# Kernel optimization log

Measured on AMD Instinct MI355X. Metric: run time of the kernel, lower is better.

The kernel has to match this reference:

```python
import jax, jax.numpy as jnp
import numpy as np

B, N, NSAMPLE = 8, 2048, 32
D = 64          # input feature channels
C1, C2 = 64, 128  # MLP channels (channels list after +3 on input: 67 -> 64 -> 128)
RADIUS = 0.15
EPS = 1e-5


def setup_inputs() -> dict:
    key = jax.random.key(0)
    ks = jax.random.split(key, 4)
    position = jax.random.uniform(ks[0], (B, N, 3), dtype=jnp.float32)
    feature = jax.random.normal(ks[1], (B, N, D), dtype=jnp.float32)
    W1 = jax.random.normal(ks[2], (D + 3, C1), dtype=jnp.float32) * 0.05
    gamma1 = jnp.ones((C1,), jnp.float32)
    beta1 = jnp.zeros((C1,), jnp.float32)
    W2 = jax.random.normal(ks[3], (C1, C2), dtype=jnp.float32) * 0.05
    gamma2 = jnp.ones((C2,), jnp.float32)
    beta2 = jnp.zeros((C2,), jnp.float32)
    return {"position": position, "feature": feature,
            "W1": W1, "gamma1": gamma1, "beta1": beta1,
            "W2": W2, "gamma2": gamma2, "beta2": beta2}


def _ball_query(xyz, radius, nsample):
    # squared pairwise distances [B, N, N]
    sq = (jnp.sum(xyz ** 2, -1)[:, :, None]
          + jnp.sum(xyz ** 2, -1)[:, None, :]
          - 2.0 * jnp.einsum('bnc,bmc->bnm', xyz, xyz))
    n = xyz.shape[1]
    idx = jnp.where(sq > radius ** 2, n, jnp.arange(n, dtype=jnp.int32)[None, None, :])
    idx = jnp.sort(idx, axis=-1)[:, :, :nsample]            # [B, N, nsample]
    first = idx[:, :, :1]
    return jnp.where(idx == n, first, idx)                  # pad misses with first neighbor


def _gather(points, idx):
    # points [B, N, C], idx [B, S, K] -> [B, S, K, C]
    b, s, k = idx.shape
    flat = jnp.take_along_axis(points, idx.reshape(b, s * k, 1), axis=1)
    return flat.reshape(b, s, k, points.shape[-1])


def _bn_relu(x, gamma, beta, relu=True):
    # BatchNorm1d over channel dim (train-mode stats across B*N*S), per linearblock
    mean = jnp.mean(x, axis=(0, 1, 2), keepdims=True)
    var = jnp.var(x, axis=(0, 1, 2), keepdims=True)
    y = (x - mean) * jax.lax.rsqrt(var + EPS) * gamma + beta
    return jax.nn.relu(y) if relu else y


def reference(position, feature, W1, gamma1, beta1, W2, gamma2, beta2):
    b, n, _ = position.shape
    idx = _ball_query(position, RADIUS, NSAMPLE)            # [B, N, nsample]
    grouped_xyz = _gather(position, idx) - position[:, :, None, :]  # [B,N,ns,3]
    grouped_feat = _gather(feature, idx)                    # [B, N, ns, D]
    h = jnp.concatenate([grouped_xyz, grouped_feat], axis=-1)  # [B, N, ns, 3+D]
    h = _bn_relu(h @ W1, gamma1, beta1)                     # [B, N, ns, C1]
    h = _bn_relu(h @ W2, gamma2, beta2)                     # [B, N, ns, C2]
    new_feature = jnp.max(h, axis=2)                        # [B, N, C2]
    return position, new_feature
```

## Files before the change

kernel.cpp:

```cpp
#include <hip/hip_runtime.h>
#include <hip/hip_bf16.h>


#define BB 8
#define NN 2048
#define KK 32
#define DD 64
#define CC1 64
#define CC2 128
#define TOTROWS (BB*NN*KK)
#define SITES (BB*NN)
#define PSLICES 256
#define DBLOCKS 1024

typedef __bf16 bf16x8 __attribute__((ext_vector_type(8)));
typedef float  f32x4  __attribute__((ext_vector_type(4)));

__device__ __forceinline__ void lds_add(float* p, float v) {
  __hip_atomic_fetch_add(p, v, __ATOMIC_RELAXED, __HIP_MEMORY_SCOPE_WORKGROUP);
}

__global__ __launch_bounds__(1024, 1) void kQ_ball_scatter(
    const float* __restrict__ pos, int* __restrict__ idx,
    float* __restrict__ Pc, float* __restrict__ Px,
    float* __restrict__ Py, float* __restrict__ Pz,
    float* __restrict__ momP)
{
  __shared__ float4 P[NN];
  __shared__ unsigned int Sc[NN], Sx[NN], Sy[NN], Sz[NN];
  __shared__ int idxL[64*KK];
  __shared__ float mred[16*9];
  const int b = blockIdx.x >> 5;
  const int slice = blockIdx.x & 31;
  for (int i = threadIdx.x; i < NN; i += 1024) {
    const float* p = pos + ((size_t)b*NN + i)*3;
    float x = p[0], y = p[1], z = p[2];
    float s = __fadd_rn(__fadd_rn(__fmul_rn(x,x), __fmul_rn(y,y)), __fmul_rn(z,z));
    P[i] = make_float4(x, y, z, s);
    Sc[i] = 0u; Sx[i] = 0u; Sy[i] = 0u; Sz[i] = 0u;
  }
  __syncthreads();
  const int wave = threadIdx.x >> 6, lane = threadIdx.x & 63;
  const float R2 = (float)(0.15 * 0.15);
  const unsigned long long lt = (lane == 63) ? 0x7fffffffffffffffull
                                             : ((1ull << lane) - 1ull);
  for (int qi = wave; qi < 64; qi += 16) {
    const int q = slice*64 + qi;
    const float4 Q = P[q];
    int* ip = idx + ((size_t)b*NN + q)*KK;
    int* il = idxL + qi*KK;
    int cnt = 0, first = -1;
    for (int step = 0; step < 32; ++step) {
      float4 p = P[step*64 + lane];
      float d = __fmul_rn(Q.x, p.x);
      d = fmaf(Q.y, p.y, d);
      d = fmaf(Q.z, p.z, d);
      float sq = __fsub_rn(__fadd_rn(Q.w, p.w), __fmul_rn(2.0f, d));
      bool in = !(sq > R2);
      unsigned long long mask = __ballot(in);
      if (first < 0 && mask) first = step*64 + (int)__builtin_ctzll(mask);
      int dst = cnt + (int)__popcll(mask & lt);
      if (in && dst < KK) { ip[dst] = step*64 + lane; il[dst] = step*64 + lane; }
      cnt += (int)__popcll(mask);
      if (cnt >= KK) break;
    }
    if (lane >= cnt && lane < KK) { ip[lane] = first; il[lane] = first; }
  }
  __syncthreads();
  const int sl = threadIdx.x >> 4;
  const int kg = threadIdx.x & 15;
  const int ip0 = idxL[sl*KK];
  const float4 C = P[slice*64 + sl];
  const float FS = 4194304.0f;
  float m1x=0.f,m1y=0.f,m1z=0.f,mxx=0.f,myy=0.f,mzz=0.f,mxy=0.f,mxz=0.f,myz=0.f;
  int wt = 0;
  #pragma unroll
  for (int j = 0; j < 2; ++j) {
    const int k = kg*2 + j;
    const int m = idxL[sl*KK + k];
    const float4 Pm = P[m];
    float dx = Pm.x - C.x;
    float dy = Pm.y - C.y;
    float dz = Pm.z - C.z;
    if (k > 0 && m == ip0) {
      ++wt;
    } else {
      atomicAdd(&Sc[m], 1u);
      atomicAdd(&Sx[m], (unsigned int)__float2int_rn(dx*FS));
      atomicAdd(&Sy[m], (unsigned int)__float2int_rn(dy*FS));
      atomicAdd(&Sz[m], (unsigned int)__float2int_rn(dz*FS));
    }
    m1x += dx; m1y += dy; m1z += dz;
    mxx = fmaf(dx,dx,mxx); myy = fmaf(dy,dy,myy); mzz = fmaf(dz,dz,mzz);
    mxy = fmaf(dx,dy,mxy); mxz = fmaf(dx,dz,mxz); myz = fmaf(dy,dz,myz);
  }
  if (wt > 0) {
    const float4 P0 = P[ip0];
    float dx0 = P0.x - C.x;
    float dy0 = P0.y - C.y;
    float dz0 = P0.z - C.z;
    atomicAdd(&Sc[ip0], (unsigned int)wt);
    atomicAdd(&Sx[ip0], (unsigned int)(wt*__float2int_rn(dx0*FS)));
    atomicAdd(&Sy[ip0], (unsigned int)(wt*__float2int_rn(dy0*FS)));
    atomicAdd(&Sz[ip0], (unsigned int)(wt*__float2int_rn(dz0*FS)));
  }
  const int wv = threadIdx.x >> 6;
  float vals[9] = {m1x,m1y,m1z,mxx,myy,mzz,mxy,mxz,myz};
  #pragma unroll
  for (int i = 0; i < 9; ++i) {
    float v = vals[i];
    #pragma unroll
    for (int s = 1; s < 64; s <<= 1) v += __shfl_xor(v, s, 64);
    if (lane == 0) mred[wv*9 + i] = v;
  }
  __syncthreads();
  const float IS = 2.38418579101562500e-7f;
  float* pc = Pc + (size_t)blockIdx.x*NN;
  float* px = Px + (size_t)blockIdx.x*NN;
  float* py = Py + (size_t)blockIdx.x*NN;
  float* pz = Pz + (size_t)blockIdx.x*NN;
  for (int i = threadIdx.x; i < NN; i += 1024) {
    pc[i] = (float)Sc[i];
    px[i] = (float)(int)Sx[i] * IS;
    py[i] = (float)(int)Sy[i] * IS;
    pz[i] = (float)(int)Sz[i] * IS;
  }
  if (threadIdx.x < 9) {
    float s = 0.f;
    #pragma unroll
    for (int w2 = 0; w2 < 16; ++w2) s += mred[w2*9 + threadIdx.x];
    momP[(size_t)blockIdx.x*16 + threadIdx.x] = s;
  }
}

__global__ __launch_bounds__(256) void kB_g(const float* __restrict__ feat,
                                            const float* __restrict__ W1,
                                            const float* __restrict__ Pc,
                                            const float* __restrict__ Px,
                                            const float* __restrict__ Py,
                                            const float* __restrict__ Pz,
                                            float* __restrict__ g,
                                            float* __restrict__ A_p)
{
  __shared__ float red[320];
  __shared__ float cntL[128], dxL[128], dyL[128], dzL[128];
  for (int i = threadIdx.x; i < 320; i += 256) red[i] = 0.f;
  const int row0B = blockIdx.x * 128;
  const int bb = row0B >> 11;
  for (int r2 = threadIdx.x; r2 < 128; r2 += 256) {
    const int m = (row0B + r2) & (NN-1);
    float s0 = 0.f, s1 = 0.f, s2 = 0.f, s3 = 0.f;
    #pragma unroll 4
    for (int q = 0; q < 32; ++q) {
      const size_t base = (size_t)(bb*32 + q)*NN + m;
      s0 += Pc[base]; s1 += Px[base]; s2 += Py[base]; s3 += Pz[base];
    }
    cntL[r2] = s0; dxL[r2] = s1; dyL[r2] = s2; dzL[r2] = s3;
  }
  __syncthreads();
  const int lane = threadIdx.x & 63;
  const int quad = lane >> 4;
  const int col  = lane & 15;
  const int gw = (blockIdx.x*256 + threadIdx.x) >> 6;

  bf16x8 Bf[2][4];
  #pragma unroll
  for (int kt = 0; kt < 2; ++kt)
    #pragma unroll
    for (int nt = 0; nt < 4; ++nt) {
      bf16x8 v;
      #pragma unroll
      for (int j = 0; j < 8; ++j)
        v[j] = (__bf16)W1[(3 + kt*32 + quad*8 + j)*CC1 + nt*16 + col];
      Bf[kt][nt] = v;
    }
  float a1[4], a2[4], a3[4], a4[4], a5[4];
  #pragma unroll
  for (int nt = 0; nt < 4; ++nt) { a1[nt]=0.f; a2[nt]=0.f; a3[nt]=0.f; a4[nt]=0.f; a5[nt]=0.f; }

  for (int t = 0; t < 2; ++t) {
    const int row0 = (gw*2 + t) * 16;
    bf16x8 Af[2];
    #pragma unroll
    for (int kt = 0; kt < 2; ++kt) {
      const float4* fp =
        (const float4*)(feat + (size_t)(row0 + col)*DD + kt*32 + quad*8);
      float4 f0 = fp[0], f1 = fp[1];
      float fv[8] = {f0.x,f0.y,f0.z,f0.w,f1.x,f1.y,f1.z,f1.w};
      bf16x8 v;
      #pragma unroll
      for (int j = 0; j < 8; ++j) v[j] = (__bf16)fv[j];
      Af[kt] = v;
    }
    float cw[4], dxw[4], dyw[4], dzw[4];
    #pragma unroll
    for (int r = 0; r < 4; ++r) {
      int rl = row0 - row0B + quad*4 + r;
      cw[r] = cntL[rl]; dxw[r] = dxL[rl]; dyw[r] = dyL[rl]; dzw[r] = dzL[rl];
    }
    #pragma unroll
    for (int nt = 0; nt < 4; ++nt) {
      f32x4 a = {0.f, 0.f, 0.f, 0.f};
      a = __builtin_amdgcn_mfma_f32_16x16x32_bf16(Af[0], Bf[0][nt], a, 0, 0, 0);
      a = __builtin_amdgcn_mfma_f32_16x16x32_bf16(Af[1], Bf[1][nt], a, 0, 0, 0);
      #pragma unroll
      for (int r = 0; r < 4; ++r) {
        float v = a[r];
        g[(size_t)(row0 + quad*4 + r)*CC1 + nt*16 + col] = v;
        float cv = cw[r]*v;
        a1[nt] += cv; a2[nt] = fmaf(cv, v, a2[nt]);
        a3[nt] = fmaf(dxw[r], v, a3[nt]);
        a4[nt] = fmaf(dyw[r], v, a4[nt]);
        a5[nt] = fmaf(dzw[r], v, a5[nt]);
      }
    }
  }
  #pragma unroll
  for (int nt = 0; nt < 4; ++nt) {
    float v1=a1[nt], v2=a2[nt], v3=a3[nt], v4=a4[nt], v5=a5[nt];
    v1 += __shfl_xor(v1,16,64); v1 += __shfl_xor(v1,32,64);
    v2 += __shfl_xor(v2,16,64); v2 += __shfl_xor(v2,32,64);
    v3 += __shfl_xor(v3,16,64); v3 += __shfl_xor(v3,32,64);
    v4 += __shfl_xor(v4,16,64); v4 += __shfl_xor(v4,32,64);
    v5 += __shfl_xor(v5,16,64); v5 += __shfl_xor(v5,32,64);
    if (quad == 0) {
      int ch = nt*16 + col;
      lds_add(&red[ch], v1);
      lds_add(&red[64+ch], v2);
      lds_add(&red[128+ch], v3);
      lds_add(&red[192+ch], v4);
      lds_add(&red[256+ch], v5);
    }
  }
  __syncthreads();
  for (int i = threadIdx.x; i < 320; i += 256)
    A_p[(size_t)blockIdx.x*320 + i] = red[i];
}

__global__ __launch_bounds__(256) void kS_fold(
    const float* __restrict__ W1, const float* __restrict__ gamma1,
    const float* __restrict__ beta1, const float* __restrict__ A_p,
    const float* __restrict__ momP,
    float* __restrict__ sc1, float* __restrict__ sh1, float* __restrict__ W1s)
{
  __shared__ float AL[320];
  __shared__ float mr[256];
  __shared__ float momL[16];
  {
    const int t = threadIdx.x;
    const int i = t & 15, jq = t >> 4;
    float s = 0.f;
    #pragma unroll
    for (int q = 0; q < 16; ++q) s += momP[(size_t)(jq*16 + q)*16 + i];
    mr[t] = s;
  }
  for (int c = threadIdx.x; c < 320; c += 256) {
    float s = 0.f;
    for (int blk = 0; blk < 128; ++blk) s += A_p[(size_t)blk*320 + c];
    AL[c] = s;
  }
  __syncthreads();
  if (threadIdx.x < 16) {
    float tot = 0.f;
    #pragma unroll
    for (int q = 0; q < 16; ++q) tot += mr[q*16 + threadIdx.x];
    momL[threadIdx.x] = tot;
  }
  __syncthreads();
  const int c = threadIdx.x;
  if (c >= CC1) return;
  float wx = W1[c], wy = W1[CC1+c], wz = W1[2*CC1+c];
  float A1 = AL[c], A2 = AL[64+c];
  float A3x = AL[128+c], A3y = AL[192+c], A3z = AL[256+c];
  float sum1 = A1 + wx*momL[0] + wy*momL[1] + wz*momL[2];
  float ss = A2 + 2.f*(wx*A3x + wy*A3y + wz*A3z)
           + wx*wx*momL[3] + wy*wy*momL[4] + wz*wz*momL[5]
           + 2.f*(wx*wy*momL[6] + wx*wz*momL[7] + wy*wz*momL[8]);
  const float invN = 1.0f / (float)TOTROWS;
  float mean = sum1 * invN;
  float var  = ss * invN - mean*mean;
  float sc = rsqrtf(var + 1e-5f) * gamma1[c];
  float sh = beta1[c] - mean * sc;
  sc1[c] = sc; sh1[c] = sh;
  W1s[c] = wx*sc; W1s[64+c] = wy*sc; W1s[128+c] = wz*sc;
}

__global__ __launch_bounds__(256, 2) void kD_mfma(
    const float* __restrict__ pos, const int* __restrict__ idx,
    const float* __restrict__ g, const float* __restrict__ sc1,
    const float* __restrict__ sh1, const float* __restrict__ W1s,
    const float* __restrict__ W2,
    float* __restrict__ stats2P, float* __restrict__ out_nf)
{
  __shared__ __bf16 W2T[CC2*72];
  __shared__ float red2[256];
  red2[threadIdx.x] = 0.f;
  {
    const int n  = threadIdx.x & 127;
    const int k0 = (threadIdx.x >> 7) << 5;
    #pragma unroll
    for (int jj = 0; jj < 4; ++jj) {
      unsigned int pk[4];
      #pragma unroll
      for (int q2 = 0; q2 < 4; ++q2) {
        const int k = k0 + jj*8 + q2*2;
        __bf16 lo = (__bf16)W2[(size_t)k*CC2 + n];
        __bf16 hi = (__bf16)W2[(size_t)(k+1)*CC2 + n];
        unsigned short ulo, uhi;
        __builtin_memcpy(&ulo, &lo, 2);
        __builtin_memcpy(&uhi, &hi, 2);
        pk[q2] = ((unsigned int)uhi << 16) | (unsigned int)ulo;
      }
      __builtin_memcpy(&W2T[n*72 + k0 + jj*8], pk, 16);
    }
  }
  __syncthreads();

  const int lane = threadIdx.x & 63;
  const int quad = lane >> 4;
  const int col  = lane & 15;
  const int wv = (blockIdx.x*256 + threadIdx.x) >> 6;

  float ssum[8], ssq[8];
  #pragma unroll
  for (int nt = 0; nt < 8; ++nt) { ssum[nt] = 0.f; ssq[nt] = 0.f; }

  #pragma clang loop unroll(disable)
  for (int si = 0; si < 4; ++si) {
    const int site = wv*4 + si;
    const int b  = site >> 11;
    const int ls = site & (NN-1);
    const float* pb = pos + (size_t)b*NN*3;
    const int* ip = idx + (size_t)site*KK;

    const int ma = ip[col], mb = ip[16 + col];
    const float ccx = pb[ls*3], ccy = pb[ls*3+1], ccz = pb[ls*3+2];
    const float dxa = pb[ma*3]-ccx, dya = pb[ma*3+1]-ccy, dza = pb[ma*3+2]-ccz;
    const float dxb = pb[mb*3]-ccx, dyb = pb[mb*3+1]-ccy, dzb = pb[mb*3+2]-ccz;

    const float* gbase = g + (size_t)b*NN*CC1;
    const float* ra = gbase + (size_t)ma*CC1 + quad*8;
    const float* rb = gbase + (size_t)mb*CC1 + quad*8;
    f32x4 gA0 = *(const f32x4*)ra,      gA1 = *(const f32x4*)(ra+4);
    f32x4 gA2 = *(const f32x4*)(ra+32), gA3 = *(const f32x4*)(ra+36);
    f32x4 gB0 = *(const f32x4*)rb,      gB1 = *(const f32x4*)(rb+4);
    f32x4 gB2 = *(const f32x4*)(rb+32), gB3 = *(const f32x4*)(rb+36);

    bf16x8 A00, A01, A10, A11;
    {
      const int c0 = quad*8;
      f32x4 x0 = *(const f32x4*)&W1s[c0],     x1 = *(const f32x4*)&W1s[c0+4];
      f32x4 y0 = *(const f32x4*)&W1s[64+c0],  y1 = *(const f32x4*)&W1s[64+c0+4];
      f32x4 z0 = *(const f32x4*)&W1s[128+c0], z1 = *(const f32x4*)&W1s[128+c0+4];
      f32x4 s0 = *(const f32x4*)&sc1[c0],     s1 = *(const f32x4*)&sc1[c0+4];
      f32x4 h0 = *(const f32x4*)&sh1[c0],     h1 = *(const f32x4*)&sh1[c0+4];
      #pragma unroll
      for (int j = 0; j < 8; ++j) {
        float wx = (j<4)?x0[j]:x1[j-4], wy = (j<4)?y0[j]:y1[j-4];
        float wz = (j<4)?z0[j]:z1[j-4], sc = (j<4)?s0[j]:s1[j-4];
        float sh = (j<4)?h0[j]:h1[j-4];
        float ga = (j<4)?gA0[j]:gA1[j-4], gb = (j<4)?gB0[j]:gB1[j-4];
        float ta = fmaf(dza, wz, fmaf(dya, wy, fmaf(dxa, wx, sh)));
        A00[j] = (__bf16)fmaxf(fmaf(ga, sc, ta), 0.f);
        float tb = fmaf(dzb, wz, fmaf(dyb, wy, fmaf(dxb, wx, sh)));
        A10[j] = (__bf16)fmaxf(fmaf(gb, sc, tb), 0.f);
      }
    }
    {
      const int c0 = 32 + quad*8;
      f32x4 x0 = *(const f32x4*)&W1s[c0],     x1 = *(const f32x4*)&W1s[c0+4];
      f32x4 y0 = *(const f32x4*)&W1s[64+c0],  y1 = *(const f32x4*)&W1s[64+c0+4];
      f32x4 z0 = *(const f32x4*)&W1s[128+c0], z1 = *(const f32x4*)&W1s[128+c0+4];
      f32x4 s0 = *(const f32x4*)&sc1[c0],     s1 = *(const f32x4*)&sc1[c0+4];
      f32x4 h0 = *(const f32x4*)&sh1[c0],     h1 = *(const f32x4*)&sh1[c0+4];
      #pragma unroll
      for (int j = 0; j < 8; ++j) {
        float wx = (j<4)?x0[j]:x1[j-4], wy = (j<4)?y0[j]:y1[j-4];
        float wz = (j<4)?z0[j]:z1[j-4], sc = (j<4)?s0[j]:s1[j-4];
        float sh = (j<4)?h0[j]:h1[j-4];
        float ga = (j<4)?gA2[j]:gA3[j-4], gb = (j<4)?gB2[j]:gB3[j-4];
        float ta = fmaf(dza, wz, fmaf(dya, wy, fmaf(dxa, wx, sh)));
        A01[j] = (__bf16)fmaxf(fmaf(ga, sc, ta), 0.f);
        float tb = fmaf(dzb, wz, fmaf(dyb, wy, fmaf(dxb, wx, sh)));
        A11[j] = (__bf16)fmaxf(fmaf(gb, sc, tb), 0.f);
      }
    }

    float* outp = out_nf + (size_t)site*CC2;
    #pragma unroll
    for (int nt = 0; nt < 8; ++nt) {
      const bf16x8 B0 = *(const bf16x8*)&W2T[(nt*16 + col)*72 + quad*8];
      const bf16x8 B1 = *(const bf16x8*)&W2T[(nt*16 + col)*72 + 32 + quad*8];
      float mxv = -3.0e38f;
      f32x4 a = {0.f, 0.f, 0.f, 0.f};
      a = __builtin_amdgcn_mfma_f32_16x16x32_bf16(A00, B0, a, 0, 0, 0);
      a = __builtin_amdgcn_mfma_f32_16x16x32_bf16(A01, B1, a, 0, 0, 0);
      #pragma unroll
      for (int r = 0; r < 4; ++r) {
        float v = a[r];
        ssum[nt] += v; ssq[nt] = fmaf(v, v, ssq[nt]); mxv = fmaxf(mxv, v);
      }
      f32x4 a2 = {0.f, 0.f, 0.f, 0.f};
      a2 = __builtin_amdgcn_mfma_f32_16x16x32_bf16(A10, B0, a2, 0, 0, 0);
      a2 = __builtin_amdgcn_mfma_f32_16x16x32_bf16(A11, B1, a2, 0, 0, 0);
      #pragma unroll
      for (int r = 0; r < 4; ++r) {
        float v = a2[r];
        ssum[nt] += v; ssq[nt] = fmaf(v, v, ssq[nt]); mxv = fmaxf(mxv, v);
      }
      mxv = fmaxf(mxv, __shfl_xor(mxv, 16, 64));
      mxv = fmaxf(mxv, __shfl_xor(mxv, 32, 64));
      if ((nt & 3) == quad) outp[nt*16 + col] = mxv;
    }
  }

  #pragma unroll
  for (int nt = 0; nt < 8; ++nt) {
    float s = ssum[nt];
    s += __shfl_xor(s, 16, 64); s += __shfl_xor(s, 32, 64);
    float q = ssq[nt];
    q += __shfl_xor(q, 16, 64); q += __shfl_xor(q, 32, 64);
    if (lane < 16) {
      atomicAdd(&red2[nt*16 + col], s);
      atomicAdd(&red2[128 + nt*16 + col], q);
    }
  }
  __syncthreads();
  stats2P[(size_t)blockIdx.x*256 + threadIdx.x] = red2[threadIdx.x];
}

__global__ __launch_bounds__(256) void kR2_stats(
    const float* __restrict__ stats2P, float* __restrict__ stats2)
{
  __shared__ float r[256];
  const int c = blockIdx.x;
  float s = 0.f;
  for (int i = threadIdx.x; i < DBLOCKS; i += 256)
    s += stats2P[(size_t)i*256 + c];
  r[threadIdx.x] = s;
  __syncthreads();
  for (int off = 128; off > 0; off >>= 1) {
    if (threadIdx.x < off) r[threadIdx.x] += r[threadIdx.x + off];
    __syncthreads();
  }
  if (threadIdx.x == 0) stats2[c] = r[0];
}

__global__ __launch_bounds__(256) void k45_epi(const float* __restrict__ pos,
                                               const float* __restrict__ g2,
                                               const float* __restrict__ be2,
                                               const float* __restrict__ stats2,
                                               float* __restrict__ out)
{
  int i = blockIdx.x*256 + threadIdx.x;
  if (blockIdx.x < 192) { out[i] = pos[i]; return; }
  int j = i - 192*256;
  int c = j & (CC2-1);
  const float invc = 1.0f / (float)TOTROWS;
  float mean = stats2[c] * invc;
  float var  = stats2[128 + c] * invc - mean*mean;
  float sc = rsqrtf(var + 1e-5f) * g2[c];
  float sh = be2[c] - mean * sc;
  float* out_nf = out + (size_t)BB*NN*3;
  float x = out_nf[j];
  out_nf[j] = fmaxf(fmaf(x, sc, sh), 0.f);
}

extern "C" void kernel_launch(void* const* d_in, const int* in_sizes, int n_in,
                              void* d_out, int out_size, void* d_ws, size_t ws_size,
                              hipStream_t stream) {
  const float* pos  = (const float*)d_in[0];
  const float* feat = (const float*)d_in[1];
  const float* W1   = (const float*)d_in[2];
  const float* g1   = (const float*)d_in[3];
  const float* be1  = (const float*)d_in[4];
  const float* W2   = (const float*)d_in[5];
  const float* g2   = (const float*)d_in[6];
  const float* be2  = (const float*)d_in[7];
  float* out = (float*)d_out;
  float* out_nf = out + (size_t)BB*NN*3;

  char* w = (char*)d_ws;
  int*   idx    = (int*)w;
  float* stats2 = (float*)(w + 0x200000);
  float* sc1    = stats2 + 256;
  float* sh1    = sc1 + 64;
  float* W1s    = sh1 + 64;
  float* A_p    = (float*)(w + 0x210000);
  float* momP   = (float*)(w + 0x250000);
  float* Pc     = (float*)(w + 0x260000);
  float* Px     = Pc + (size_t)PSLICES*NN;
  float* Py     = Px + (size_t)PSLICES*NN;
  float* Pz     = Py + (size_t)PSLICES*NN;
  float* stats2P= (float*)(w + 0x660000);
  float* g      = (float*)(w + 0xA60000);

  kQ_ball_scatter<<<256, 1024, 0, stream>>>(pos, idx, Pc, Px, Py, Pz, momP);
  kB_g      <<<128, 256, 0, stream>>>(feat, W1, Pc, Px, Py, Pz, g, A_p);
  kS_fold   <<<1, 256, 0, stream>>>(W1, g1, be1, A_p, momP, sc1, sh1, W1s);
  kD_mfma   <<<DBLOCKS, 256, 0, stream>>>(pos, idx, g, sc1, sh1, W1s, W2,
                                          stats2P, out_nf);
  kR2_stats <<<256, 256, 0, stream>>>(stats2P, stats2);
  k45_epi   <<<192 + (SITES*CC2)/256, 256, 0, stream>>>(pos, g2, be2, stats2, out);
}
```

Baseline: 173.6 us.

## Fold BN reduction kernels into consumers and move position copy into ball query

Removes the single-block kS_fold kernel by having every kD_mfma block redundantly reduce A_p and momP and compute the layer-1 BN scale/shift into LDS. It also removes kR2_stats: each epilogue block re-reduces all 1024 stats2P partials itself, then applies BN2+ReLU with float4 accesses. The position passthrough copy moves into kQ_ball_scatter. This cuts two launches and their serial dependencies, but each block now does redundant global reads of the partial sums (about 40K floats per kD block and 256K per epilogue block).

```diff
diff --git a/kernel.cpp b/kernel.cpp
--- a/kernel.cpp
+++ b/kernel.cpp
@@ -24,7 +24,7 @@
     const float* __restrict__ pos, int* __restrict__ idx,
     float* __restrict__ Pc, float* __restrict__ Px,
     float* __restrict__ Py, float* __restrict__ Pz,
-    float* __restrict__ momP)
+    float* __restrict__ momP, float* __restrict__ out)
 {
   __shared__ float4 P[NN];
   __shared__ unsigned int Sc[NN], Sx[NN], Sy[NN], Sz[NN];
@@ -131,6 +131,8 @@
     for (int w2 = 0; w2 < 16; ++w2) s += mred[w2*9 + threadIdx.x];
     momP[(size_t)blockIdx.x*16 + threadIdx.x] = s;
   }
+  if (threadIdx.x < 192)
+    out[blockIdx.x*192 + threadIdx.x] = pos[blockIdx.x*192 + threadIdx.x];
 }
 
 __global__ __launch_bounds__(256) void kB_g(const float* __restrict__ feat,
@@ -237,63 +239,21 @@
     A_p[(size_t)blockIdx.x*320 + i] = red[i];
 }
 
-__global__ __launch_bounds__(256) void kS_fold(
-    const float* __restrict__ W1, const float* __restrict__ gamma1,
-    const float* __restrict__ beta1, const float* __restrict__ A_p,
-    const float* __restrict__ momP,
-    float* __restrict__ sc1, float* __restrict__ sh1, float* __restrict__ W1s)
-{
-  __shared__ float AL[320];
-  __shared__ float mr[256];
-  __shared__ float momL[16];
-  {
-    const int t = threadIdx.x;
-    const int i = t & 15, jq = t >> 4;
-    float s = 0.f;
-    #pragma unroll
-    for (int q = 0; q < 16; ++q) s += momP[(size_t)(jq*16 + q)*16 + i];
-    mr[t] = s;
-  }
-  for (int c = threadIdx.x; c < 320; c += 256) {
-    float s = 0.f;
-    for (int blk = 0; blk < 128; ++blk) s += A_p[(size_t)blk*320 + c];
-    AL[c] = s;
-  }
-  __syncthreads();
-  if (threadIdx.x < 16) {
-    float tot = 0.f;
-    #pragma unroll
-    for (int q = 0; q < 16; ++q) tot += mr[q*16 + threadIdx.x];
-    momL[threadIdx.x] = tot;
-  }
-  __syncthreads();
-  const int c = threadIdx.x;
-  if (c >= CC1) return;
-  float wx = W1[c], wy = W1[CC1+c], wz = W1[2*CC1+c];
-  float A1 = AL[c], A2 = AL[64+c];
-  float A3x = AL[128+c], A3y = AL[192+c], A3z = AL[256+c];
-  float sum1 = A1 + wx*momL[0] + wy*momL[1] + wz*momL[2];
-  float ss = A2 + 2.f*(wx*A3x + wy*A3y + wz*A3z)
-           + wx*wx*momL[3] + wy*wy*momL[4] + wz*wz*momL[5]
-           + 2.f*(wx*wy*momL[6] + wx*wz*momL[7] + wy*wz*momL[8]);
-  const float invN = 1.0f / (float)TOTROWS;
-  float mean = sum1 * invN;
-  float var  = ss * invN - mean*mean;
-  float sc = rsqrtf(var + 1e-5f) * gamma1[c];
-  float sh = beta1[c] - mean * sc;
-  sc1[c] = sc; sh1[c] = sh;
-  W1s[c] = wx*sc; W1s[64+c] = wy*sc; W1s[128+c] = wz*sc;
-}
-
 __global__ __launch_bounds__(256, 2) void kD_mfma(
     const float* __restrict__ pos, const int* __restrict__ idx,
-    const float* __restrict__ g, const float* __restrict__ sc1,
-    const float* __restrict__ sh1, const float* __restrict__ W1s,
+    const float* __restrict__ g, const float* __restrict__ A_p,
+    const float* __restrict__ momP, const float* __restrict__ W1,
+    const float* __restrict__ gamma1, const float* __restrict__ beta1,
     const float* __restrict__ W2,
     float* __restrict__ stats2P, float* __restrict__ out_nf)
 {
   __shared__ __bf16 W2T[CC2*72];
   __shared__ float red2[256];
+  __shared__ alignas(16) float AL[320];
+  __shared__ float momL[16];
+  __shared__ alignas(16) float sc1L[64];
+  __shared__ alignas(16) float sh1L[64];
+  __shared__ alignas(16) float W1sL[192];
   red2[threadIdx.x] = 0.f;
   {
     const int n  = threadIdx.x & 127;
@@ -314,6 +274,34 @@
       __builtin_memcpy(&W2T[n*72 + k0 + jj*8], pk, 16);
     }
   }
+  for (int c = threadIdx.x; c < 320; c += 256) {
+    float s = 0.f;
+    for (int blk = 0; blk < 128; ++blk) s += A_p[(size_t)blk*320 + c];
+    AL[c] = s;
+  }
+  if (threadIdx.x < 16) {
+    float s = 0.f;
+    for (int q = 0; q < PSLICES; ++q) s += momP[(size_t)q*16 + threadIdx.x];
+    momL[threadIdx.x] = s;
+  }
+  __syncthreads();
+  if (threadIdx.x < CC1) {
+    const int c = threadIdx.x;
+    float wx = W1[c], wy = W1[CC1+c], wz = W1[2*CC1+c];
+    float A1 = AL[c], A2 = AL[64+c];
+    float A3x = AL[128+c], A3y = AL[192+c], A3z = AL[256+c];
+    float sum1 = A1 + wx*momL[0] + wy*momL[1] + wz*momL[2];
+    float ss = A2 + 2.f*(wx*A3x + wy*A3y + wz*A3z)
+             + wx*wx*momL[3] + wy*wy*momL[4] + wz*wz*momL[5]
+             + 2.f*(wx*wy*momL[6] + wx*wz*momL[7] + wy*wz*momL[8]);
+    const float invN = 1.0f / (float)TOTROWS;
+    float mean = sum1 * invN;
+    float var  = ss * invN - mean*mean;
+    float sc = rsqrtf(var + 1e-5f) * gamma1[c];
+    float sh = beta1[c] - mean * sc;
+    sc1L[c] = sc; sh1L[c] = sh;
+    W1sL[c] = wx*sc; W1sL[64+c] = wy*sc; W1sL[128+c] = wz*sc;
+  }
   __syncthreads();
 
   const int lane = threadIdx.x & 63;
@@ -349,11 +337,11 @@
     bf16x8 A00, A01, A10, A11;
     {
       const int c0 = quad*8;
-      f32x4 x0 = *(const f32x4*)&W1s[c0],     x1 = *(const f32x4*)&W1s[c0+4];
-      f32x4 y0 = *(const f32x4*)&W1s[64+c0],  y1 = *(const f32x4*)&W1s[64+c0+4];
-      f32x4 z0 = *(const f32x4*)&W1s[128+c0], z1 = *(const f32x4*)&W1s[128+c0+4];
-      f32x4 s0 = *(const f32x4*)&sc1[c0],     s1 = *(const f32x4*)&sc1[c0+4];
-      f32x4 h0 = *(const f32x4*)&sh1[c0],     h1 = *(const f32x4*)&sh1[c0+4];
+      f32x4 x0 = *(const f32x4*)&W1sL[c0],     x1 = *(const f32x4*)&W1sL[c0+4];
+      f32x4 y0 = *(const f32x4*)&W1sL[64+c0],  y1 = *(const f32x4*)&W1sL[64+c0+4];
+      f32x4 z0 = *(const f32x4*)&W1sL[128+c0], z1 = *(const f32x4*)&W1sL[128+c0+4];
+      f32x4 s0 = *(const f32x4*)&sc1L[c0],     s1 = *(const f32x4*)&sc1L[c0+4];
+      f32x4 h0 = *(const f32x4*)&sh1L[c0],     h1 = *(const f32x4*)&sh1L[c0+4];
       #pragma unroll
       for (int j = 0; j < 8; ++j) {
         float wx = (j<4)?x0[j]:x1[j-4], wy = (j<4)?y0[j]:y1[j-4];
@@ -368,11 +356,11 @@
     }
     {
       const int c0 = 32 + quad*8;
-      f32x4 x0 = *(const f32x4*)&W1s[c0],     x1 = *(const f32x4*)&W1s[c0+4];
-      f32x4 y0 = *(const f32x4*)&W1s[64+c0],  y1 = *(const f32x4*)&W1s[64+c0+4];
-      f32x4 z0 = *(const f32x4*)&W1s[128+c0], z1 = *(const f32x4*)&W1s[128+c0+4];
-      f32x4 s0 = *(const f32x4*)&sc1[c0],     s1 = *(const f32x4*)&sc1[c0+4];
-      f32x4 h0 = *(const f32x4*)&sh1[c0],     h1 = *(const f32x4*)&sh1[c0+4];
+      f32x4 x0 = *(const f32x4*)&W1sL[c0],     x1 = *(const f32x4*)&W1sL[c0+4];
+      f32x4 y0 = *(const f32x4*)&W1sL[64+c0],  y1 = *(const f32x4*)&W1sL[64+c0+4];
+      f32x4 z0 = *(const f32x4*)&W1sL[128+c0], z1 = *(const f32x4*)&W1sL[128+c0+4];
+      f32x4 s0 = *(const f32x4*)&sc1L[c0],     s1 = *(const f32x4*)&sc1L[c0+4];
+      f32x4 h0 = *(const f32x4*)&sh1L[c0],     h1 = *(const f32x4*)&sh1L[c0+4];
       #pragma unroll
       for (int j = 0; j < 8; ++j) {
         float wx = (j<4)?x0[j]:x1[j-4], wy = (j<4)?y0[j]:y1[j-4];
@@ -429,41 +417,40 @@
   stats2P[(size_t)blockIdx.x*256 + threadIdx.x] = red2[threadIdx.x];
 }
 
-__global__ __launch_bounds__(256) void kR2_stats(
-    const float* __restrict__ stats2P, float* __restrict__ stats2)
+__global__ __launch_bounds__(256) void k45_epi(
+    const float* __restrict__ stats2P, const float* __restrict__ g2,
+    const float* __restrict__ be2, float* __restrict__ out)
 {
-  __shared__ float r[256];
-  const int c = blockIdx.x;
-  float s = 0.f;
-  for (int i = threadIdx.x; i < DBLOCKS; i += 256)
-    s += stats2P[(size_t)i*256 + c];
-  r[threadIdx.x] = s;
-  __syncthreads();
-  for (int off = 128; off > 0; off >>= 1) {
-    if (threadIdx.x < off) r[threadIdx.x] += r[threadIdx.x + off];
-    __syncthreads();
-  }
-  if (threadIdx.x == 0) stats2[c] = r[0];
-}
-
-__global__ __launch_bounds__(256) void k45_epi(const float* __restrict__ pos,
-                                               const float* __restrict__ g2,
-                                               const float* __restrict__ be2,
-                                               const float* __restrict__ stats2,
-                                               float* __restrict__ out)
-{
-  int i = blockIdx.x*256 + threadIdx.x;
-  if (blockIdx.x < 192) { out[i] = pos[i]; return; }
-  int j = i - 192*256;
-  int c = j & (CC2-1);
-  const float invc = 1.0f / (float)TOTROWS;
-  float mean = stats2[c] * invc;
-  float var  = stats2[128 + c] * invc - mean*mean;
-  float sc = rsqrtf(var + 1e-5f) * g2[c];
-  float sh = be2[c] - mean * sc;
+  __shared__ float stF[256];
+  __shared__ float scL[128], shL[128];
+  const int t = threadIdx.x;
+  {
+    float s = 0.f;
+    for (int blk = 0; blk < DBLOCKS; ++blk)
+      s += stats2P[(size_t)blk*256 + t];
+    stF[t] = s;
+  }
+  __syncthreads();
+  if (t < CC2) {
+    const float invc = 1.0f / (float)TOTROWS;
+    float mean = stF[t] * invc;
+    float var  = stF[128 + t] * invc - mean*mean;
+    float sc = rsqrtf(var + 1e-5f) * g2[t];
+    scL[t] = sc; shL[t] = be2[t] - mean * sc;
+  }
+  __syncthreads();
   float* out_nf = out + (size_t)BB*NN*3;
-  float x = out_nf[j];
-  out_nf[j] = fmaxf(fmaf(x, sc, sh), 0.f);
+  float4* o4 = (float4*)out_nf;
+  const size_t e0 = (size_t)blockIdx.x * 2048;
+  for (int e = t; e < 2048; e += 256) {
+    float4 x = o4[e0 + e];
+    const int c = (e << 2) & (CC2-1);
+    x.x = fmaxf(fmaf(x.x, scL[c  ], shL[c  ]), 0.f);
+    x.y = fmaxf(fmaf(x.y, scL[c+1], shL[c+1]), 0.f);
+    x.z = fmaxf(fmaf(x.z, scL[c+2], shL[c+2]), 0.f);
+    x.w = fmaxf(fmaf(x.w, scL[c+3], shL[c+3]), 0.f);
+    o4[e0 + e] = x;
+  }
 }
 
 extern "C" void kernel_launch(void* const* d_in, const int* in_sizes, int n_in,
@@ -482,10 +469,6 @@
 
   char* w = (char*)d_ws;
   int*   idx    = (int*)w;
-  float* stats2 = (float*)(w + 0x200000);
-  float* sc1    = stats2 + 256;
-  float* sh1    = sc1 + 64;
-  float* W1s    = sh1 + 64;
   float* A_p    = (float*)(w + 0x210000);
   float* momP   = (float*)(w + 0x250000);
   float* Pc     = (float*)(w + 0x260000);
@@ -495,11 +478,9 @@
   float* stats2P= (float*)(w + 0x660000);
   float* g      = (float*)(w + 0xA60000);
 
-  kQ_ball_scatter<<<256, 1024, 0, stream>>>(pos, idx, Pc, Px, Py, Pz, momP);
+  kQ_ball_scatter<<<256, 1024, 0, stream>>>(pos, idx, Pc, Px, Py, Pz, momP, out);
   kB_g      <<<128, 256, 0, stream>>>(feat, W1, Pc, Px, Py, Pz, g, A_p);
-  kS_fold   <<<1, 256, 0, stream>>>(W1, g1, be1, A_p, momP, sc1, sh1, W1s);
-  kD_mfma   <<<DBLOCKS, 256, 0, stream>>>(pos, idx, g, sc1, sh1, W1s, W2,
-                                          stats2P, out_nf);
-  kR2_stats <<<256, 256, 0, stream>>>(stats2P, stats2);
-  k45_epi   <<<192 + (SITES*CC2)/256, 256, 0, stream>>>(pos, g2, be2, stats2, out);
-}
+  kD_mfma   <<<DBLOCKS, 256, 0, stream>>>(pos, idx, g, A_p, momP,
+                                          W1, g1, be1, W2, stats2P, out_nf);
+  k45_epi   <<<256, 256, 0, stream>>>(stats2P, g2, be2, out);
+}
```

Measured after the change: 203.3 us. 17.1% more time.

## Fuse BN2 stats reduction into epilogue and move position copy into ball kernel

Applied to the files above, without the earlier changes.

Removes the separate stats-reduction kernel: every epilogue block now reduces all per-block partial stats itself, computes scale/shift into LDS, then applies BN+ReLU with float4 vectorized accesses. The position passthrough copy is moved into the ball-query kernel. This saves a launch and the intermediate stats buffer, but makes each of 256 blocks redundantly read the full 1 MB partial-stats array serially.

```diff
diff --git a/kernel.cpp b/kernel.cpp
--- a/kernel.cpp
+++ b/kernel.cpp
@@ -24,7 +24,7 @@
     const float* __restrict__ pos, int* __restrict__ idx,
     float* __restrict__ Pc, float* __restrict__ Px,
     float* __restrict__ Py, float* __restrict__ Pz,
-    float* __restrict__ momP)
+    float* __restrict__ momP, float* __restrict__ out)
 {
   __shared__ float4 P[NN];
   __shared__ unsigned int Sc[NN], Sx[NN], Sy[NN], Sz[NN];
@@ -131,6 +131,8 @@
     for (int w2 = 0; w2 < 16; ++w2) s += mred[w2*9 + threadIdx.x];
     momP[(size_t)blockIdx.x*16 + threadIdx.x] = s;
   }
+  if (threadIdx.x < 192)
+    out[blockIdx.x*192 + threadIdx.x] = pos[blockIdx.x*192 + threadIdx.x];
 }
 
 __global__ __launch_bounds__(256) void kB_g(const float* __restrict__ feat,
@@ -429,41 +431,40 @@
   stats2P[(size_t)blockIdx.x*256 + threadIdx.x] = red2[threadIdx.x];
 }
 
-__global__ __launch_bounds__(256) void kR2_stats(
-    const float* __restrict__ stats2P, float* __restrict__ stats2)
+__global__ __launch_bounds__(256) void k45_epi(
+    const float* __restrict__ stats2P, const float* __restrict__ g2,
+    const float* __restrict__ be2, float* __restrict__ out)
 {
-  __shared__ float r[256];
-  const int c = blockIdx.x;
-  float s = 0.f;
-  for (int i = threadIdx.x; i < DBLOCKS; i += 256)
-    s += stats2P[(size_t)i*256 + c];
-  r[threadIdx.x] = s;
-  __syncthreads();
-  for (int off = 128; off > 0; off >>= 1) {
-    if (threadIdx.x < off) r[threadIdx.x] += r[threadIdx.x + off];
-    __syncthreads();
-  }
-  if (threadIdx.x == 0) stats2[c] = r[0];
-}
-
-__global__ __launch_bounds__(256) void k45_epi(const float* __restrict__ pos,
-                                               const float* __restrict__ g2,
-                                               const float* __restrict__ be2,
-                                               const float* __restrict__ stats2,
-                                               float* __restrict__ out)
-{
-  int i = blockIdx.x*256 + threadIdx.x;
-  if (blockIdx.x < 192) { out[i] = pos[i]; return; }
-  int j = i - 192*256;
-  int c = j & (CC2-1);
-  const float invc = 1.0f / (float)TOTROWS;
-  float mean = stats2[c] * invc;
-  float var  = stats2[128 + c] * invc - mean*mean;
-  float sc = rsqrtf(var + 1e-5f) * g2[c];
-  float sh = be2[c] - mean * sc;
+  __shared__ float stF[256];
+  __shared__ float scL[128], shL[128];
+  const int t = threadIdx.x;
+  {
+    float s = 0.f;
+    for (int blk = 0; blk < DBLOCKS; ++blk)
+      s += stats2P[(size_t)blk*256 + t];
+    stF[t] = s;
+  }
+  __syncthreads();
+  if (t < CC2) {
+    const float invc = 1.0f / (float)TOTROWS;
+    float mean = stF[t] * invc;
+    float var  = stF[128 + t] * invc - mean*mean;
+    float sc = rsqrtf(var + 1e-5f) * g2[t];
+    scL[t] = sc; shL[t] = be2[t] - mean * sc;
+  }
+  __syncthreads();
   float* out_nf = out + (size_t)BB*NN*3;
-  float x = out_nf[j];
-  out_nf[j] = fmaxf(fmaf(x, sc, sh), 0.f);
+  float4* o4 = (float4*)out_nf;
+  const size_t e0 = (size_t)blockIdx.x * 2048;
+  for (int e = t; e < 2048; e += 256) {
+    float4 x = o4[e0 + e];
+    const int c = (e << 2) & (CC2-1);
+    x.x = fmaxf(fmaf(x.x, scL[c  ], shL[c  ]), 0.f);
+    x.y = fmaxf(fmaf(x.y, scL[c+1], shL[c+1]), 0.f);
+    x.z = fmaxf(fmaf(x.z, scL[c+2], shL[c+2]), 0.f);
+    x.w = fmaxf(fmaf(x.w, scL[c+3], shL[c+3]), 0.f);
+    o4[e0 + e] = x;
+  }
 }
 
 extern "C" void kernel_launch(void* const* d_in, const int* in_sizes, int n_in,
@@ -482,8 +483,7 @@
 
   char* w = (char*)d_ws;
   int*   idx    = (int*)w;
-  float* stats2 = (float*)(w + 0x200000);
-  float* sc1    = stats2 + 256;
+  float* sc1    = (float*)(w + 0x200000);
   float* sh1    = sc1 + 64;
   float* W1s    = sh1 + 64;
   float* A_p    = (float*)(w + 0x210000);
@@ -495,11 +495,10 @@
   float* stats2P= (float*)(w + 0x660000);
   float* g      = (float*)(w + 0xA60000);
 
-  kQ_ball_scatter<<<256, 1024, 0, stream>>>(pos, idx, Pc, Px, Py, Pz, momP);
+  kQ_ball_scatter<<<256, 1024, 0, stream>>>(pos, idx, Pc, Px, Py, Pz, momP, out);
   kB_g      <<<128, 256, 0, stream>>>(feat, W1, Pc, Px, Py, Pz, g, A_p);
   kS_fold   <<<1, 256, 0, stream>>>(W1, g1, be1, A_p, momP, sc1, sh1, W1s);
   kD_mfma   <<<DBLOCKS, 256, 0, stream>>>(pos, idx, g, sc1, sh1, W1s, W2,
                                           stats2P, out_nf);
-  kR2_stats <<<256, 256, 0, stream>>>(stats2P, stats2);
-  k45_epi   <<<192 + (SITES*CC2)/256, 256, 0, stream>>>(pos, g2, be2, stats2, out);
-}
+  k45_epi   <<<256, 256, 0, stream>>>(stats2P, g2, be2, out);
+}
```

Result: slower. 195.0 us (+12.3%).
